# Optimization experiments

Hardware: AMD Instinct MI355X
Metric: run time of the kernel (lower is better)

## Reference

```python
import jax, jax.numpy as jnp
import numpy as np

HEADS = 8

def setup_inputs() -> dict:
    key = jax.random.key(0)
    k1, k2, k3 = jax.random.split(key, 3)
    B, C, L = 8, 512, 4096
    dim_head = 64
    hidden = HEADS * dim_head  # 512
    x = jax.random.normal(k1, (B, C, L), dtype=jnp.float32)
    # Conv1d(dim, hidden*3, 1, bias=False) -> weight [hidden*3, dim]
    w_qkv = jax.random.normal(k2, (hidden * 3, C), dtype=jnp.float32) * 0.02
    # Conv1d(hidden, dim, 1) -> weight [dim, hidden], bias [dim]
    w_out = jax.random.normal(k3, (C, hidden), dtype=jnp.float32) * 0.02
    b_out = jnp.zeros((C,), dtype=jnp.float32)
    return {"x": x, "w_qkv": w_qkv, "w_out": w_out, "b_out": b_out}

def reference(x, w_qkv, w_out, b_out):
    B, C, L = x.shape
    # 1x1 Conv1d == channel matmul
    qkv = jnp.einsum('oc,bcl->bol', w_qkv, x)            # [B, 3*H*dh, L]
    qkv = qkv.reshape(B, 3, HEADS, -1, L)                # qkv outermost, then heads, then c
    q, k, v = qkv[:, 0], qkv[:, 1], qkv[:, 2]            # each [B, H, dh, L]
    k = jax.nn.softmax(k, axis=-1)                       # softmax over sequence
    context = jnp.einsum('bhdn,bhen->bhde', k, v)        # [B, H, dh, dh]
    out = jnp.einsum('bhde,bhdn->bhen', context, q)      # [B, H, dh, L]
    out = out.reshape(B, -1, L)                          # [B, H*dh, L]
    return jnp.einsum('oc,bcl->bol', w_out, out) + b_out[None, :, None]
```

## Files before the change

kernel.cpp:

```cpp
#include <hip/hip_runtime.h>
#include <hip/hip_bf16.h>


typedef __bf16 bf16x8 __attribute__((ext_vector_type(8)));
typedef __bf16 bf16x4 __attribute__((ext_vector_type(4)));
typedef float  f32x4  __attribute__((ext_vector_type(4)));

#define B_  8
#define L_  4096
#define C_  512

#define GLD_LDS16(g, l)                                             \
    __builtin_amdgcn_global_load_lds(                               \
        (const __attribute__((address_space(1))) void*)(g),         \
        (__attribute__((address_space(3))) void*)(l), 16, 0, 0)

#define FENCE asm volatile("" ::: "memory")
#define BAR   do { FENCE; __builtin_amdgcn_s_barrier(); FENCE; } while (0)
#define DRAIN_LGKM asm volatile("s_waitcnt lgkmcnt(0)" ::: "memory")
#define WAIT_VM(N) asm volatile("s_waitcnt vmcnt(" #N ")" ::: "memory")

__global__ __launch_bounds__(256) void prep_all(const float* __restrict__ x,
                                                __hip_bfloat16* __restrict__ xt,
                                                const float* __restrict__ wqkv_f,
                                                __hip_bfloat16* __restrict__ wkv_b,
                                                __hip_bfloat16* __restrict__ wqT) {
    __shared__ float tile[64 * 133];
    int blk = blockIdx.x;
    int t = threadIdx.x;
    if (blk < 2048) {
        int b = blk >> 8, rem = blk & 255;
        int l0 = (rem & 31) * 128, c0 = (rem >> 5) * 64;
        const float* xp = x + ((size_t)b * C_ + c0) * L_ + l0;
#pragma unroll
        for (int p = 0; p < 8; p++) {
            int i = p * 8 + (t >> 5);
            int j = (t & 31) * 4;
            float4 vv = *(const float4*)(xp + (size_t)i * L_ + j);
            *(float4*)&tile[i * 133 + j] = vv;
        }
        __syncthreads();
        unsigned short* xo = (unsigned short*)xt + ((size_t)b * L_ + l0) * C_ + c0;
#pragma unroll
        for (int qq = 0; qq < 8; qq++) {
            int l = qq * 16 + (t >> 4);
            int cg = (t & 15) * 4;
            bf16x4 ov;
#pragma unroll
            for (int k = 0; k < 4; k++) ov[k] = (__bf16)tile[(cg + k) * 133 + l];
            *(bf16x4*)(xo + (size_t)l * C_ + cg) = ov;
        }
    } else if (blk < 4096) {
        int i = (blk - 2048) * 256 + t;
        wkv_b[i] = __float2bfloat16(wqkv_f[512 * 512 + i]);
    } else {
        int tb = blk - 4096;
        int r0 = (tb >> 4) * 32, c0 = (tb & 15) * 32;
        int tx = t & 31, ty = t >> 5;
        for (int r = 0; r < 32; r += 8)
            tile[(ty + r) * 33 + tx] = wqkv_f[(size_t)(r0 + ty + r) * 512 + c0 + tx];
        __syncthreads();
        for (int r = 0; r < 32; r += 8)
            wqT[(size_t)(c0 + ty + r) * 512 + r0 + tx] = __float2bfloat16(tile[tx * 33 + ty + r]);
    }
}

template <int MODE>
__global__ __launch_bounds__(256, 2) void gemm_p(
    const __hip_bfloat16* __restrict__ A, const __hip_bfloat16* __restrict__ Bt,
    size_t strideA, size_t strideB, int M, int N, int K,
    __hip_bfloat16* __restrict__ kb, __hip_bfloat16* __restrict__ vb,
    __hip_bfloat16* __restrict__ obf,
    float* __restrict__ outb, const float* __restrict__ bias) {
    __shared__ alignas(16) unsigned short sA[2][128 * 64];
    __shared__ alignas(16) unsigned short sB[2][128 * 64];

    int b = blockIdx.z;
    int m0 = blockIdx.y * 128, n0 = blockIdx.x * 128;
    const __hip_bfloat16* Ab = A + strideA * (size_t)b;
    const __hip_bfloat16* Bb = Bt + strideB * (size_t)b;

    int t = threadIdx.x;
    int lane = t & 63, wv = t >> 6;
    int l16 = lane & 15, q4 = lane >> 4;
    int wr = (wv >> 1) * 64, wc = (wv & 1) * 64;

    int srow = lane >> 3;
    int swz  = ((lane & 7) ^ srow) * 8;

    const __hip_bfloat16* gA[4];
    const __hip_bfloat16* gB[4];
    unsigned ldoff[4];
#pragma unroll
    for (int c = 0; c < 4; c++) {
        int r = c * 32 + wv * 8;
        gA[c] = Ab + (size_t)(m0 + r + srow) * K + swz;
        gB[c] = Bb + (size_t)(n0 + r + srow) * K + swz;
        ldoff[c] = (unsigned)r * 64;
    }

    int gsel0 = (q4 ^ (l16 & 7)) * 8;
    int gsel1 = gsel0 ^ 32;
    unsigned rA = (unsigned)(wr + l16) * 64;
    unsigned rB = (unsigned)(wc + l16) * 64;
    int NKT = K >> 6;

    f32x4 acc[4][4] = {};
    bf16x8 aF[4][2], bF[4][2];

#pragma unroll
    for (int c = 0; c < 4; c++) GLD_LDS16(gA[c], &sA[0][ldoff[c]]);
#pragma unroll
    for (int c = 0; c < 4; c++) GLD_LDS16(gB[c], &sB[0][ldoff[c]]);
    if (NKT > 1) {
#pragma unroll
        for (int c = 0; c < 4; c++) GLD_LDS16(gA[c] + 64, &sA[1][ldoff[c]]);
        WAIT_VM(4);
    } else {
        WAIT_VM(0);
    }
    BAR;

#pragma unroll 1
    for (int kt = 0; kt < NKT; ++kt) {
        int cur = kt & 1, nbuf = cur ^ 1;
        const unsigned short* As_b = sA[cur];
        const unsigned short* Bs_b = sB[cur];
        bool st1 = (kt + 1) < NKT;
        bool st2 = (kt + 2) < NKT;

#pragma unroll
        for (int i = 0; i < 4; i++) {
            aF[i][0] = *(const bf16x8*)&As_b[rA + i * 1024 + gsel0];
            aF[i][1] = *(const bf16x8*)&As_b[rA + i * 1024 + gsel1];
        }
#pragma unroll
        for (int j = 0; j < 2; j++) {
            bF[j][0] = *(const bf16x8*)&Bs_b[rB + j * 1024 + gsel0];
            bF[j][1] = *(const bf16x8*)&Bs_b[rB + j * 1024 + gsel1];
        }
        if (st1) {
            int ko = (kt + 1) << 6;
#pragma unroll
            for (int c = 0; c < 4; c++) GLD_LDS16(gB[c] + ko, &sB[nbuf][ldoff[c]]);
        }
        BAR;
        __builtin_amdgcn_s_setprio(1);
#pragma unroll
        for (int ks = 0; ks < 2; ks++)
#pragma unroll
            for (int i = 0; i < 4; i++)
#pragma unroll
                for (int j = 0; j < 2; j++)
                    acc[i][j] = __builtin_amdgcn_mfma_f32_16x16x32_bf16(aF[i][ks], bF[j][ks], acc[i][j], 0, 0, 0);
        __builtin_amdgcn_s_setprio(0);
        DRAIN_LGKM;
        BAR;

#pragma unroll
        for (int j = 2; j < 4; j++) {
            bF[j][0] = *(const bf16x8*)&Bs_b[rB + j * 1024 + gsel0];
            bF[j][1] = *(const bf16x8*)&Bs_b[rB + j * 1024 + gsel1];
        }
        if (st2) {
            int ko = (kt + 2) << 6;
#pragma unroll
            for (int c = 0; c < 4; c++) GLD_LDS16(gA[c] + ko, &sA[cur][ldoff[c]]);
        }
        BAR;
        __builtin_amdgcn_s_setprio(1);
#pragma unroll
        for (int ks = 0; ks < 2; ks++)
#pragma unroll
            for (int i = 0; i < 4; i++)
#pragma unroll
                for (int j = 0; j < 2; j++)
                    acc[i][2 + j] = __builtin_amdgcn_mfma_f32_16x16x32_bf16(aF[i][ks], bF[2 + j][ks], acc[i][2 + j], 0, 0, 0);
        __builtin_amdgcn_s_setprio(0);
        DRAIN_LGKM;
        if (st2) { WAIT_VM(4); } else { WAIT_VM(0); }
        BAR;
    }

#pragma unroll
    for (int i = 0; i < 4; i++)
#pragma unroll
        for (int j = 0; j < 4; j++)
#pragma unroll
            for (int r = 0; r < 4; r++) {
                int row = m0 + wr + i * 16 + q4 * 4 + r;
                int col = n0 + wc + j * 16 + l16;
                float val = acc[i][j][r];
                if (MODE == 1) {
                    bool isk = (m0 < 512);
                    __hip_bfloat16* dst = isk ? kb : vb;
                    if (isk) val = __expf(val);
                    dst[((size_t)b * 512 + (row & 511)) * (size_t)N + col] = __float2bfloat16(val);
                } else if (MODE == 3) {
                    obf[((size_t)b * 512 + row) * (size_t)N + col] = __float2bfloat16(val);
                } else {
                    outb[((size_t)b * M + row) * (size_t)N + col] = val + bias[row];
                }
            }
}

__global__ __launch_bounds__(256) void ctx_kernel(const __hip_bfloat16* __restrict__ ek,
                                                  const __hip_bfloat16* __restrict__ v,
                                                  float* __restrict__ ctxp,
                                                  float* __restrict__ Sp) {
    int kc = blockIdx.x, h = blockIdx.y, b = blockIdx.z;
    int t = threadIdx.x, lane = t & 63, wv = t >> 6;
    int l16 = lane & 15, q4 = lane >> 4;
    const __hip_bfloat16* ka = ek + ((size_t)b * 512 + h * 64) * L_;
    const __hip_bfloat16* va = v + ((size_t)b * 512 + h * 64) * L_;

    f32x4 acc[4][4] = {};
    float ps[4] = {0.f, 0.f, 0.f, 0.f};
    int nbase = kc * 512 + wv * 128;
#pragma unroll
    for (int s = 0; s < 4; s++) {
        int n = nbase + s * 32 + q4 * 8;
        bf16x8 af[4], bfr[4];
#pragma unroll
        for (int i = 0; i < 4; i++) {
            af[i]  = *(const bf16x8*)(ka + (size_t)(i * 16 + l16) * L_ + n);
            bfr[i] = *(const bf16x8*)(va + (size_t)(i * 16 + l16) * L_ + n);
#pragma unroll
            for (int e = 0; e < 8; e++) ps[i] += (float)af[i][e];
        }
#pragma unroll
        for (int i = 0; i < 4; i++)
#pragma unroll
            for (int j = 0; j < 4; j++)
                acc[i][j] = __builtin_amdgcn_mfma_f32_16x16x32_bf16(af[i], bfr[j], acc[i][j], 0, 0, 0);
    }

    __shared__ float sred[4][64];
#pragma unroll
    for (int i = 0; i < 4; i++) {
        ps[i] += __shfl_xor(ps[i], 16, 64);
        ps[i] += __shfl_xor(ps[i], 32, 64);
    }
    if (q4 == 0) {
#pragma unroll
        for (int i = 0; i < 4; i++) sred[wv][i * 16 + l16] = ps[i];
    }

    __shared__ float cbuf[4096];
    __syncthreads();
    for (int w = 0; w < 4; w++) {
        if (wv == w) {
#pragma unroll
            for (int i = 0; i < 4; i++)
#pragma unroll
                for (int j = 0; j < 4; j++)
#pragma unroll
                    for (int r = 0; r < 4; r++) {
                        int mm = i * 16 + q4 * 4 + r, nn = j * 16 + l16;
                        float pv = acc[i][j][r];
                        if (w == 0) cbuf[mm * 64 + nn] = pv;
                        else        cbuf[mm * 64 + nn] += pv;
                    }
        }
        __syncthreads();
    }
    float* cg = ctxp + ((size_t)kc * 64 + b * 8 + h) * 4096;
    for (int i = t; i < 4096; i += 256) cg[i] = cbuf[i];
    if (t < 64)
        Sp[((size_t)kc * 64 + b * 8 + h) * 64 + t] = sred[0][t] + sred[1][t] + sred[2][t] + sred[3][t];
}

__global__ __launch_bounds__(256) void w2_kernel(const float* __restrict__ wout,
                                                 const float* __restrict__ ctxp,
                                                 const float* __restrict__ Sp,
                                                 __hip_bfloat16* __restrict__ w2) {
    int ob = blockIdx.x, h = blockIdx.y, b = blockIdx.z;
    __shared__ float cT[64 * 65];
    __shared__ float wT[64 * 65];
    __shared__ float Sinv[64];
    int t = threadIdx.x;
    const size_t SL = (size_t)64 * 4096;
    const float* cg = ctxp + ((size_t)b * 8 + h) * 4096;
    if (t < 64) {
        const float* sg = Sp + ((size_t)b * 8 + h) * 64;
        float S = 0.f;
#pragma unroll
        for (int s = 0; s < 8; s++) S += sg[(size_t)s * 64 * 64 + t];
        Sinv[t] = 1.0f / S;
    }
    __syncthreads();
    for (int i = t; i < 4096; i += 256) {
        int d = i >> 6, e = i & 63;
        float s = 0.f;
#pragma unroll
        for (int sl = 0; sl < 8; sl++) s += cg[(size_t)sl * SL + i];
        cT[e * 65 + d] = s * Sinv[d];
        wT[e * 65 + d] = wout[(size_t)(ob * 64 + d) * 512 + h * 64 + e];
    }
    __syncthreads();
    int ol = t >> 2;
    int db = (t & 3) * 16;
    unsigned short* w2p = (unsigned short*)w2 + ((size_t)b * 512 + ob * 64 + ol) * 512 + h * 64;
    for (int g = 0; g < 4; g++) {
        int d0 = db + g * 4;
        float s0 = 0.f, s1 = 0.f, s2 = 0.f, s3 = 0.f;
#pragma unroll
        for (int e = 0; e < 64; e++) {
            float w = wT[e * 65 + ol];
            s0 += w * cT[e * 65 + d0];
            s1 += w * cT[e * 65 + d0 + 1];
            s2 += w * cT[e * 65 + d0 + 2];
            s3 += w * cT[e * 65 + d0 + 3];
        }
        bf16x4 ov;
        ov[0] = (__bf16)s0; ov[1] = (__bf16)s1; ov[2] = (__bf16)s2; ov[3] = (__bf16)s3;
        *(bf16x4*)(w2p + d0) = ov;
    }
}

extern "C" void kernel_launch(void* const* d_in, const int* in_sizes, int n_in,
                              void* d_out, int out_size, void* d_ws, size_t ws_size,
                              hipStream_t stream) {
    const float* x     = (const float*)d_in[0];
    const float* w_qkv = (const float*)d_in[1];
    const float* w_out = (const float*)d_in[2];
    const float* b_out = (const float*)d_in[3];
    float* out = (float*)d_out;
    char* ws = (char*)d_ws;

    const size_t QKV = (size_t)B_ * 512 * L_;
    size_t off_xt   = 0;
    size_t off_wkv  = off_xt + (size_t)B_ * L_ * C_ * 2;
    size_t off_wqT  = off_wkv + (size_t)1024 * 512 * 2;
    size_t off_k    = off_wqT + (size_t)512 * 512 * 2;
    size_t off_v    = off_k + QKV * 2;
    size_t off_ctxp = off_v + QKV * 2;
    size_t off_Sp   = off_ctxp + (size_t)8 * 64 * 4096 * 4;
    size_t off_w2   = off_k;
    size_t off_w3   = off_k + (size_t)B_ * 512 * 512 * 2;

    __hip_bfloat16* xt   = (__hip_bfloat16*)(ws + off_xt);
    __hip_bfloat16* wkvb = (__hip_bfloat16*)(ws + off_wkv);
    __hip_bfloat16* wqT  = (__hip_bfloat16*)(ws + off_wqT);
    __hip_bfloat16* kb   = (__hip_bfloat16*)(ws + off_k);
    __hip_bfloat16* vb   = (__hip_bfloat16*)(ws + off_v);
    float*          ctxp = (float*)(ws + off_ctxp);
    float*          Sp   = (float*)(ws + off_Sp);
    __hip_bfloat16* w2   = (__hip_bfloat16*)(ws + off_w2);
    __hip_bfloat16* W3   = (__hip_bfloat16*)(ws + off_w3);

    prep_all<<<4352, 256, 0, stream>>>(x, xt, w_qkv, wkvb, wqT);

    gemm_p<1><<<dim3(L_ / 128, 1024 / 128, B_), 256, 0, stream>>>(
        wkvb, xt, 0, (size_t)L_ * C_, 1024, L_, 512, kb, vb, nullptr, nullptr, nullptr);

    ctx_kernel<<<dim3(8, 8, B_), 256, 0, stream>>>(kb, vb, ctxp, Sp);

    w2_kernel<<<dim3(8, 8, B_), 256, 0, stream>>>(w_out, ctxp, Sp, w2);

    gemm_p<3><<<dim3(512 / 128, 512 / 128, B_), 256, 0, stream>>>(
        w2, wqT, (size_t)512 * 512, 0, 512, 512, 512, nullptr, nullptr, W3, nullptr, nullptr);

    gemm_p<2><<<dim3(L_ / 128, 512 / 128, B_), 256, 0, stream>>>(
        W3, xt, (size_t)512 * 512, (size_t)L_ * C_, 512, L_, 512, nullptr, nullptr, nullptr, out, b_out);
}
```

Baseline: 243.8 us.

## Widen xt stores, split ctx kernel over d halves, vectorize w2 loads

The transpose in prep_all now writes 8 bf16 values per thread with 16-byte stores instead of 4-value stores. ctx_kernel is split into two blocks per (chunk, head, batch), each handling half of the key dimension, which doubles the grid to 1024 blocks and halves the per-block accumulator and LDS use. V is now loaded twice across the two blocks. w2_kernel reads the partial contexts and w_out with float4 loads instead of scalar loads.

```diff
diff --git a/kernel.cpp b/kernel.cpp
--- a/kernel.cpp
+++ b/kernel.cpp
@@ -41,14 +41,14 @@
         }
         __syncthreads();
         unsigned short* xo = (unsigned short*)xt + ((size_t)b * L_ + l0) * C_ + c0;
-#pragma unroll
-        for (int qq = 0; qq < 8; qq++) {
-            int l = qq * 16 + (t >> 4);
-            int cg = (t & 15) * 4;
-            bf16x4 ov;
-#pragma unroll
-            for (int k = 0; k < 4; k++) ov[k] = (__bf16)tile[(cg + k) * 133 + l];
-            *(bf16x4*)(xo + (size_t)l * C_ + cg) = ov;
+        int cg8 = (t & 7) * 8;
+#pragma unroll
+        for (int qq = 0; qq < 4; qq++) {
+            int l = qq * 32 + (t >> 3);
+            bf16x8 ov;
+#pragma unroll
+            for (int k = 0; k < 8; k++) ov[k] = (__bf16)tile[(cg8 + k) * 133 + l];
+            *(bf16x8*)(xo + (size_t)l * C_ + cg8) = ov;
         }
     } else if (blk < 4096) {
         int i = (blk - 2048) * 256 + t;
@@ -208,50 +208,54 @@
                                                   const __hip_bfloat16* __restrict__ v,
                                                   float* __restrict__ ctxp,
                                                   float* __restrict__ Sp) {
-    int kc = blockIdx.x, h = blockIdx.y, b = blockIdx.z;
+    int bx = blockIdx.x;
+    int kc = bx >> 1, dh = bx & 1;
+    int h = blockIdx.y, b = blockIdx.z;
     int t = threadIdx.x, lane = t & 63, wv = t >> 6;
     int l16 = lane & 15, q4 = lane >> 4;
-    const __hip_bfloat16* ka = ek + ((size_t)b * 512 + h * 64) * L_;
+    const __hip_bfloat16* ka = ek + ((size_t)b * 512 + h * 64 + dh * 32) * L_;
     const __hip_bfloat16* va = v + ((size_t)b * 512 + h * 64) * L_;
 
-    f32x4 acc[4][4] = {};
-    float ps[4] = {0.f, 0.f, 0.f, 0.f};
+    f32x4 acc[2][4] = {};
+    float ps[2] = {0.f, 0.f};
     int nbase = kc * 512 + wv * 128;
 #pragma unroll
     for (int s = 0; s < 4; s++) {
         int n = nbase + s * 32 + q4 * 8;
-        bf16x8 af[4], bfr[4];
-#pragma unroll
-        for (int i = 0; i < 4; i++) {
-            af[i]  = *(const bf16x8*)(ka + (size_t)(i * 16 + l16) * L_ + n);
-            bfr[i] = *(const bf16x8*)(va + (size_t)(i * 16 + l16) * L_ + n);
+        bf16x8 af[2], bfr[4];
+#pragma unroll
+        for (int i = 0; i < 2; i++) {
+            af[i] = *(const bf16x8*)(ka + (size_t)(i * 16 + l16) * L_ + n);
 #pragma unroll
             for (int e = 0; e < 8; e++) ps[i] += (float)af[i][e];
         }
 #pragma unroll
-        for (int i = 0; i < 4; i++)
+        for (int j = 0; j < 4; j++)
+            bfr[j] = *(const bf16x8*)(va + (size_t)(j * 16 + l16) * L_ + n);
+#pragma unroll
+        for (int i = 0; i < 2; i++)
 #pragma unroll
             for (int j = 0; j < 4; j++)
                 acc[i][j] = __builtin_amdgcn_mfma_f32_16x16x32_bf16(af[i], bfr[j], acc[i][j], 0, 0, 0);
     }
 
-    __shared__ float sred[4][64];
-#pragma unroll
-    for (int i = 0; i < 4; i++) {
+    __shared__ float sred[4][32];
+#pragma unroll
+    for (int i = 0; i < 2; i++) {
         ps[i] += __shfl_xor(ps[i], 16, 64);
         ps[i] += __shfl_xor(ps[i], 32, 64);
     }
     if (q4 == 0) {
 #pragma unroll
-        for (int i = 0; i < 4; i++) sred[wv][i * 16 + l16] = ps[i];
-    }
-
-    __shared__ float cbuf[4096];
+        for (int i = 0; i < 2; i++) sred[wv][i * 16 + l16] = ps[i];
+    }
+
+    __shared__ float cbuf[2048];
     __syncthreads();
     for (int w = 0; w < 4; w++) {
         if (wv == w) {
 #pragma unroll
-            for (int i = 0; i < 4; i++)
+            for (int i = 0; i < 2; i++)
 #pragma unroll
                 for (int j = 0; j < 4; j++)
 #pragma unroll
@@ -264,10 +268,11 @@
         }
         __syncthreads();
     }
-    float* cg = ctxp + ((size_t)kc * 64 + b * 8 + h) * 4096;
-    for (int i = t; i < 4096; i += 256) cg[i] = cbuf[i];
-    if (t < 64)
-        Sp[((size_t)kc * 64 + b * 8 + h) * 64 + t] = sred[0][t] + sred[1][t] + sred[2][t] + sred[3][t];
+    float* cg = ctxp + ((size_t)kc * 64 + b * 8 + h) * 4096 + dh * 2048;
+    for (int i = t; i < 2048; i += 256) cg[i] = cbuf[i];
+    if (t < 32)
+        Sp[((size_t)kc * 64 + b * 8 + h) * 64 + dh * 32 + t] =
+            sred[0][t] + sred[1][t] + sred[2][t] + sred[3][t];
 }
 
 __global__ __launch_bounds__(256) void w2_kernel(const float* __restrict__ wout,
@@ -289,13 +294,26 @@
         Sinv[t] = 1.0f / S;
     }
     __syncthreads();
-    for (int i = t; i < 4096; i += 256) {
-        int d = i >> 6, e = i & 63;
-        float s = 0.f;
-#pragma unroll
-        for (int sl = 0; sl < 8; sl++) s += cg[(size_t)sl * SL + i];
-        cT[e * 65 + d] = s * Sinv[d];
-        wT[e * 65 + d] = wout[(size_t)(ob * 64 + d) * 512 + h * 64 + e];
+#pragma unroll
+    for (int it = 0; it < 4; ++it) {
+        int i0 = (t + it * 256) * 4;
+        int d = i0 >> 6, e0 = i0 & 63;
+        float4 s4 = {0.f, 0.f, 0.f, 0.f};
+#pragma unroll
+        for (int sl = 0; sl < 8; sl++) {
+            float4 vv = *(const float4*)&cg[(size_t)sl * SL + i0];
+            s4.x += vv.x; s4.y += vv.y; s4.z += vv.z; s4.w += vv.w;
+        }
+        float si = Sinv[d];
+        float4 wv4 = *(const float4*)&wout[(size_t)(ob * 64 + d) * 512 + h * 64 + e0];
+        cT[(e0 + 0) * 65 + d] = s4.x * si;
+        cT[(e0 + 1) * 65 + d] = s4.y * si;
+        cT[(e0 + 2) * 65 + d] = s4.z * si;
+        cT[(e0 + 3) * 65 + d] = s4.w * si;
+        wT[(e0 + 0) * 65 + d] = wv4.x;
+        wT[(e0 + 1) * 65 + d] = wv4.y;
+        wT[(e0 + 2) * 65 + d] = wv4.z;
+        wT[(e0 + 3) * 65 + d] = wv4.w;
     }
     __syncthreads();
     int ol = t >> 2;
@@ -354,7 +372,7 @@
     gemm_p<1><<<dim3(L_ / 128, 1024 / 128, B_), 256, 0, stream>>>(
         wkvb, xt, 0, (size_t)L_ * C_, 1024, L_, 512, kb, vb, nullptr, nullptr, nullptr);
 
-    ctx_kernel<<<dim3(8, 8, B_), 256, 0, stream>>>(kb, vb, ctxp, Sp);
+    ctx_kernel<<<dim3(16, 8, B_), 256, 0, stream>>>(kb, vb, ctxp, Sp);
 
     w2_kernel<<<dim3(8, 8, B_), 256, 0, stream>>>(w_out, ctxp, Sp, w2);
 
```

Result: no change. 243.6 us (-0.1%).
